# Kernel optimization log

Measured on AMD Instinct MI355X. Metric: run time of the kernel, lower is better.

The kernel has to match this reference:

```python
import jax, jax.numpy as jnp
import numpy as np

NUM_GROUPS = 32
EPS = 1e-5


def group_norm(x, w, b):
    # x: [B, C, H, W]
    B, C, H, W = x.shape
    g = x.reshape(B, NUM_GROUPS, C // NUM_GROUPS, H, W)
    mu = g.mean(axis=(2, 3, 4), keepdims=True)
    var = g.var(axis=(2, 3, 4), keepdims=True)
    g = (g - mu) * jax.lax.rsqrt(var + EPS)
    x = g.reshape(B, C, H, W)
    return x * w[None, :, None, None] + b[None, :, None, None]


def conv1x1(x, w, b):
    # 1x1 conv == channel matmul; x: [B, C, H, W], w: [O, C], b: [O]
    return jnp.einsum('bchw,oc->bohw', x, w) + b[None, :, None, None]


def setup_inputs() -> dict:
    key = jax.random.key(0)
    ks = jax.random.split(key, 11)
    C = 512
    B, H, W = 4, 64, 64
    s = 1.0 / np.sqrt(C)
    return {
        'x': jax.random.normal(ks[0], (B, C, H, W), jnp.float32),
        'gn_w': jax.random.uniform(ks[1], (C,), jnp.float32, 0.5, 1.5),
        'gn_b': jax.random.normal(ks[2], (C,), jnp.float32) * 0.1,
        'wq': jax.random.normal(ks[3], (C, C), jnp.float32) * s,
        'bq': jax.random.normal(ks[4], (C,), jnp.float32) * 0.01,
        'wk': jax.random.normal(ks[5], (C, C), jnp.float32) * s,
        'bk': jax.random.normal(ks[6], (C,), jnp.float32) * 0.01,
        'wv': jax.random.normal(ks[7], (C, C), jnp.float32) * s,
        'bv': jax.random.normal(ks[8], (C,), jnp.float32) * 0.01,
        'wo': jax.random.normal(ks[9], (C, C), jnp.float32) * s,
        'bo': jax.random.normal(ks[10], (C,), jnp.float32) * 0.01,
    }


def reference(x, gn_w, gn_b, wq, bq, wk, bk, wv, bv, wo, bo):
    B, C, H, W = x.shape
    h_ = group_norm(x, gn_w, gn_b)
    q = conv1x1(h_, wq, bq).reshape(B, C, H * W)   # [B, C, HW]
    k = conv1x1(h_, wk, bk).reshape(B, C, H * W)
    v = conv1x1(h_, wv, bv).reshape(B, C, H * W)
    # scores: q^T k, scaled by C^-0.5; softmax over keys
    scores = jnp.einsum('bci,bcj->bij', q, k) * (C ** -0.5)  # [B, HW, HW]
    attn = jax.nn.softmax(scores, axis=-1)
    # h_[b,c,i] = sum_j v[b,c,j] * attn[b,i,j]
    h_ = jnp.einsum('bcj,bij->bci', v, attn).reshape(B, C, H, W)
    return x + conv1x1(h_, wo, bo)
```

## Files before the change

kernel.cpp:

```cpp
#include <hip/hip_runtime.h>
#include <hip/hip_bf16.h>

typedef __attribute__((ext_vector_type(8))) __bf16 bf16x8;
typedef __attribute__((ext_vector_type(4))) float f32x4;

__device__ __forceinline__ unsigned short f2bf(float f) {
  union { float f; unsigned u; } v; v.f = f;
  unsigned r = v.u + 0x7fffu + ((v.u >> 16) & 1u);
  return (unsigned short)(r >> 16);
}

__device__ __forceinline__ void gload_lds16(const void* g, void* s) {
  __builtin_amdgcn_global_load_lds(
      (const __attribute__((address_space(1))) void*)g,
      (__attribute__((address_space(3))) void*)s, 16, 0, 0);
}

__global__ __launch_bounds__(256) void convert_w(
    const float* __restrict__ wq, const float* __restrict__ wk,
    const float* __restrict__ wv, const float* __restrict__ wo,
    unsigned short* __restrict__ dst) {
  const int m = blockIdx.x >> 10;
  const float* src = (m == 0) ? wq : (m == 1) ? wk : (m == 2) ? wv : wo;
  const int idx = ((blockIdx.x & 1023) << 8) | threadIdx.x;
  dst[m * 262144 + idx] = f2bf(src[idx]);
}

__global__ __launch_bounds__(256) void zero_k(float* __restrict__ p, int n) {
  const int i = blockIdx.x * 256 + threadIdx.x;
  if (i < n) p[i] = 0.f;
}

__global__ __launch_bounds__(256) void gn_stats(
    const float* __restrict__ x, float2* __restrict__ partials) {
  const int bg = blockIdx.x >> 2, part = blockIdx.x & 3;
  const float* xg = x + (size_t)bg * 65536 + part * 1024;
  const int t = threadIdx.x;
  float s = 0.f, ss = 0.f;
#pragma unroll
  for (int r = 0; r < 16; ++r) {
    const float4 v = *(const float4*)(xg + (size_t)r * 4096 + t * 4);
    s += v.x + v.y + v.z + v.w;
    ss += v.x * v.x + v.y * v.y + v.z * v.z + v.w * v.w;
  }
#pragma unroll
  for (int m = 32; m; m >>= 1) { s += __shfl_xor(s, m); ss += __shfl_xor(ss, m); }
  __shared__ float red[8];
  const int wave = t >> 6, lane = t & 63;
  if (lane == 0) { red[wave] = s; red[wave + 4] = ss; }
  __syncthreads();
  if (t == 0) {
    float2 p;
    p.x = red[0] + red[1] + red[2] + red[3];
    p.y = red[4] + red[5] + red[6] + red[7];
    partials[blockIdx.x] = p;
  }
}

__global__ __launch_bounds__(256) void gn_apply(
    const float* __restrict__ x, const float2* __restrict__ partials,
    const float* __restrict__ gw, const float* __restrict__ gb,
    unsigned short* __restrict__ h_t) {
  const int bg = blockIdx.x >> 3, cc = blockIdx.x & 7;
  const int b = bg >> 5, g = bg & 31;
  const int t = threadIdx.x;
  __shared__ float chs[32];
  __shared__ unsigned short tile[16][520];
  if (t < 16) {
    const float2 p0 = partials[bg * 4 + 0], p1 = partials[bg * 4 + 1];
    const float2 p2 = partials[bg * 4 + 2], p3 = partials[bg * 4 + 3];
    const float S = p0.x + p1.x + p2.x + p3.x;
    const float SS = p0.y + p1.y + p2.y + p3.y;
    const float mu = S * (1.f / 65536.f);
    const float rstd = rsqrtf(SS * (1.f / 65536.f) - mu * mu + 1e-5f);
    const float sc = gw[g * 16 + t] * rstd;
    chs[t] = sc;
    chs[16 + t] = gb[g * 16 + t] - mu * sc;
  }
  __syncthreads();
  const float* xg = x + (size_t)bg * 65536 + cc * 512;
#pragma unroll
  for (int rr = 0; rr < 8; ++rr) {
    const int r = rr * 2 + (t >> 7), i = (t & 127) * 4;
    const float4 v = *(const float4*)(xg + (size_t)r * 4096 + i);
    const float sc = chs[r], sh = chs[16 + r];
    ushort4 o;
    o.x = f2bf(v.x * sc + sh); o.y = f2bf(v.y * sc + sh);
    o.z = f2bf(v.z * sc + sh); o.w = f2bf(v.w * sc + sh);
    *(ushort4*)&tile[r][i] = o;
  }
  __syncthreads();
  unsigned short* outp = h_t + ((size_t)b * 4096 + cc * 512) * 512 + g * 16;
#pragma unroll
  for (int rep = 0; rep < 4; ++rep) {
    const int task = rep * 256 + t;
    const int nl = task >> 1, half = (task & 1) * 8;
    ushort4 o0, o1;
    o0.x = tile[half + 0][nl]; o0.y = tile[half + 1][nl];
    o0.z = tile[half + 2][nl]; o0.w = tile[half + 3][nl];
    o1.x = tile[half + 4][nl]; o1.y = tile[half + 5][nl];
    o1.z = tile[half + 6][nl]; o1.w = tile[half + 7][nl];
    *(ushort4*)(outp + (size_t)nl * 512 + half) = o0;
    *(ushort4*)(outp + (size_t)nl * 512 + half + 4) = o1;
  }
}

__global__ __launch_bounds__(256) void reduce4_k(
    const float* __restrict__ part, const float* __restrict__ l,
    unsigned short* __restrict__ dst) {
  const size_t i = ((size_t)blockIdx.x * 256 + threadIdx.x) * 4;
  f32x4 s0 = *(const f32x4*)(part + i);
  f32x4 s1 = *(const f32x4*)(part + 2097152 + i);
  f32x4 s2 = *(const f32x4*)(part + 4194304 + i);
  f32x4 s3 = *(const f32x4*)(part + 6291456 + i);
  f32x4 s = (s0 + s1) + (s2 + s3);
  const float inv = 1.f / l[i >> 9];
  ushort4 o;
  o.x = f2bf(s[0] * inv); o.y = f2bf(s[1] * inv);
  o.z = f2bf(s[2] * inv); o.w = f2bf(s[3] * inv);
  *(ushort4*)(dst + i) = o;
}

__global__ __launch_bounds__(512, 4) void gemm_s256(
    const unsigned short* __restrict__ A, const unsigned short* __restrict__ Bt,
    unsigned short* __restrict__ Out, float* __restrict__ lsum) {
  __shared__ __align__(16) char smem[73728];
  const int tid = threadIdx.x;
  const int wave = tid >> 6, lane = tid & 63;
  const int l15 = lane & 15, l4 = lane >> 4;
  const int wm = wave >> 1, wn = wave & 1;

  const int bz = blockIdx.z;
  A += (size_t)bz * 2097152;
  Bt += (size_t)bz * 2097152;
  Out += (size_t)bz * 16777216;
  lsum += (size_t)bz * 4096;

  const int id = blockIdx.y * 32 + blockIdx.x;
  const int xcd = id & 7, j = id >> 3;
  const int by = ((xcd >> 1) << 2) + (j >> 4);
  const int bx = ((xcd & 1) << 4) + (j & 15);
  const int row0 = by << 8, col0 = bx << 7;

  const int ar = tid >> 2;
  const int akc = (tid & 3) ^ ((tid >> 3) & 3);

  auto stage = [&](int kt, int bi) {
    const int kb = kt << 5;
    char* base = smem + bi * 24576;
    const unsigned short* gA = A + (size_t)(row0 + ar) * 512 + kb + akc * 8;
    const unsigned short* gB = Bt + (size_t)(col0 + ar) * 512 + kb + akc * 8;
    gload_lds16(gA, base + wave * 1024);
    gload_lds16(gA + (size_t)128 * 512, base + 8192 + wave * 1024);
    gload_lds16(gB, base + 16384 + wave * 1024);
  };

  f32x4 acc[4][4];
#pragma unroll
  for (int r = 0; r < 4; ++r)
#pragma unroll
    for (int c = 0; c < 4; ++c) acc[r][c] = (f32x4)0.f;

  const int xsw = (l4 ^ ((l15 >> 1) & 3)) << 4;

  auto compute = [&](int bi) {
    const char* pa = smem + bi * 24576 + (wm * 64 + l15) * 64 + xsw;
    const char* pb = smem + bi * 24576 + 16384 + (wn * 64 + l15) * 64 + xsw;
    bf16x8 af[4], bfr[4];
#pragma unroll
    for (int r = 0; r < 4; ++r) af[r] = *(const bf16x8*)(pa + r * 1024);
#pragma unroll
    for (int c = 0; c < 4; ++c) bfr[c] = *(const bf16x8*)(pb + c * 1024);
#pragma unroll
    for (int r = 0; r < 4; ++r)
#pragma unroll
      for (int c = 0; c < 4; ++c)
        acc[r][c] = __builtin_amdgcn_mfma_f32_16x16x32_bf16(af[r], bfr[c], acc[r][c], 0, 0, 0);
  };

  stage(0, 0);
  stage(1, 1);
  int bi = 0;
  for (int kt = 0; kt < 15; ++kt) {
    asm volatile("s_waitcnt vmcnt(3)" ::: "memory");
    __builtin_amdgcn_s_barrier();
    __builtin_amdgcn_sched_barrier(0);
    if (kt + 2 < 16) stage(kt + 2, (kt + 2) % 3);
    compute(bi);
    bi = (bi == 2) ? 0 : bi + 1;
  }
  asm volatile("s_waitcnt vmcnt(0)" ::: "memory");
  __builtin_amdgcn_s_barrier();
  __builtin_amdgcn_sched_barrier(0);
  compute(bi);

  __syncthreads();
  unsigned short* tile = (unsigned short*)smem;
#pragma unroll
  for (int c = 0; c < 4; ++c) {
    const int coll = wn * 64 + c * 16 + l15;
#pragma unroll
    for (int r = 0; r < 4; ++r) {
      const int rowl = wm * 64 + r * 16 + l4 * 4;
#pragma unroll
      for (int j = 0; j < 4; ++j)
        tile[(rowl + j) * 136 + coll] = f2bf(__expf(acc[r][c][j]));
    }
  }
  __syncthreads();
#pragma unroll
  for (int it = 0; it < 8; ++it) {
    const int idx = it * 512 + tid;
    const int rw = idx >> 4, ch = (idx & 15) * 8;
    const uint4 vv = *(const uint4*)&tile[rw * 136 + ch];
    *(uint4*)(Out + (size_t)(row0 + rw) * 4096 + col0 + ch) = vv;
    const unsigned* uu = (const unsigned*)&vv;
    float s = 0.f;
#pragma unroll
    for (int q = 0; q < 4; ++q) {
      union { unsigned u; float f; } w;
      w.u = uu[q] << 16; s += w.f;
      w.u = uu[q] & 0xffff0000u; s += w.f;
    }
    s += __shfl_xor(s, 1); s += __shfl_xor(s, 2);
    s += __shfl_xor(s, 4); s += __shfl_xor(s, 8);
    if ((lane & 15) == 0) atomicAdd(&lsum[row0 + rw], s);
  }
}

__global__ __launch_bounds__(512, 2) void gemm_pv(
    const unsigned short* __restrict__ P, const unsigned short* __restrict__ Vt,
    unsigned short* __restrict__ Out, const float* __restrict__ lrow) {
  __shared__ __align__(16) char smem[147456];
  const int tid = threadIdx.x;
  const int wave = tid >> 6, lane = tid & 63;
  const int l15 = lane & 15, l4 = lane >> 4;
  const int wm = wave >> 1, wn = wave & 1;

  const int L = blockIdx.x + ((blockIdx.y + (blockIdx.z << 4)) << 2);
  const int xcd = L & 7, j = L >> 3;
  const int panel = xcd * 8 + (j >> 2);
  const int bx = j & 3, by = panel & 15, bz = panel >> 4;
  const int row0 = by << 8, col0 = bx << 7;
  P += (size_t)bz * 16777216;
  Vt += (size_t)bz * 2097152;
  Out += (size_t)bz * 2097152;
  lrow += bz * 4096;

  const int sr = tid >> 3;
  const int sc8 = (tid & 7) ^ (sr & 7);
  const unsigned short* gA = P + (size_t)(row0 + sr) * 4096 + sc8 * 8;
  const unsigned short* gB = Vt + (size_t)(col0 + sr) * 4096 + sc8 * 8;

  auto stA = [&](int kt, int bi, int p) {
    gload_lds16(gA + (size_t)(p << 6) * 4096 + (kt << 6),
                smem + bi * 49152 + p * 8192 + wave * 1024);
  };
  auto stB = [&](int kt, int bi, int p) {
    gload_lds16(gB + (size_t)(p << 6) * 4096 + (kt << 6),
                smem + bi * 49152 + 32768 + p * 8192 + wave * 1024);
  };

  f32x4 acc[4][4];
#pragma unroll
  for (int r = 0; r < 4; ++r)
#pragma unroll
    for (int c = 0; c < 4; ++c) acc[r][c] = (f32x4)0.f;

  const int sw0 = (l4 ^ (l15 & 7)) << 4;
  const int sw1 = ((4 + l4) ^ (l15 & 7)) << 4;
  const int arow = (wm * 64 + l15) << 7;
  const int brow = (wn * 64 + l15) << 7;

  bf16x8 bfr[4][2];

  stA(0, 0, 0); stA(0, 0, 1); stA(0, 0, 2); stA(0, 0, 3);
  stB(0, 0, 0); stB(0, 0, 1);
  stA(1, 1, 0); stA(1, 1, 1); stA(1, 1, 2); stA(1, 1, 3);
  stB(1, 1, 0); stB(1, 1, 1);
  asm volatile("s_waitcnt vmcnt(6)" ::: "memory");
  __builtin_amdgcn_s_barrier();
  __builtin_amdgcn_sched_barrier(0);

  int bi = 0;
#pragma unroll 1
  for (int kt = 0; kt < 64; ++kt) {
    const char* bufA = smem + bi * 49152;
    const char* bufB = bufA + 32768;
    const int pb = (bi + 2) % 3;
    const bool pre = (kt + 2 < 64);
    bf16x8 a0, a1;
    a0 = *(const bf16x8*)(bufA + arow + sw0);
    a1 = *(const bf16x8*)(bufA + arow + sw1);
#pragma unroll
    for (int c = 0; c < 4; ++c) {
      bfr[c][0] = *(const bf16x8*)(bufB + brow + c * 2048 + sw0);
      bfr[c][1] = *(const bf16x8*)(bufB + brow + c * 2048 + sw1);
    }
    if (pre) { stA(kt + 2, pb, 0); stA(kt + 2, pb, 1); }
    __builtin_amdgcn_s_barrier();
    asm volatile("s_waitcnt lgkmcnt(0)" ::: "memory");
    __builtin_amdgcn_sched_barrier(0);
    __builtin_amdgcn_s_setprio(1);
#pragma unroll
    for (int c = 0; c < 4; ++c) {
      acc[0][c] = __builtin_amdgcn_mfma_f32_16x16x32_bf16(a0, bfr[c][0], acc[0][c], 0, 0, 0);
      acc[0][c] = __builtin_amdgcn_mfma_f32_16x16x32_bf16(a1, bfr[c][1], acc[0][c], 0, 0, 0);
    }
    __builtin_amdgcn_s_setprio(0);
    __builtin_amdgcn_s_barrier();
    a0 = *(const bf16x8*)(bufA + arow + 2048 + sw0);
    a1 = *(const bf16x8*)(bufA + arow + 2048 + sw1);
    if (pre) { stA(kt + 2, pb, 2); stA(kt + 2, pb, 3); }
    __builtin_amdgcn_s_barrier();
    asm volatile("s_waitcnt lgkmcnt(0)" ::: "memory");
    __builtin_amdgcn_sched_barrier(0);
    __builtin_amdgcn_s_setprio(1);
#pragma unroll
    for (int c = 0; c < 4; ++c) {
      acc[1][c] = __builtin_amdgcn_mfma_f32_16x16x32_bf16(a0, bfr[c][0], acc[1][c], 0, 0, 0);
      acc[1][c] = __builtin_amdgcn_mfma_f32_16x16x32_bf16(a1, bfr[c][1], acc[1][c], 0, 0, 0);
    }
    __builtin_amdgcn_s_setprio(0);
    __builtin_amdgcn_s_barrier();
    a0 = *(const bf16x8*)(bufA + arow + 4096 + sw0);
    a1 = *(const bf16x8*)(bufA + arow + 4096 + sw1);
    if (pre) { stB(kt + 2, pb, 0); stB(kt + 2, pb, 1); }
    __builtin_amdgcn_s_barrier();
    asm volatile("s_waitcnt lgkmcnt(0)" ::: "memory");
    __builtin_amdgcn_sched_barrier(0);
    __builtin_amdgcn_s_setprio(1);
#pragma unroll
    for (int c = 0; c < 4; ++c) {
      acc[2][c] = __builtin_amdgcn_mfma_f32_16x16x32_bf16(a0, bfr[c][0], acc[2][c], 0, 0, 0);
      acc[2][c] = __builtin_amdgcn_mfma_f32_16x16x32_bf16(a1, bfr[c][1], acc[2][c], 0, 0, 0);
    }
    __builtin_amdgcn_s_setprio(0);
    __builtin_amdgcn_s_barrier();
    a0 = *(const bf16x8*)(bufA + arow + 6144 + sw0);
    a1 = *(const bf16x8*)(bufA + arow + 6144 + sw1);
    __builtin_amdgcn_s_barrier();
    asm volatile("s_waitcnt lgkmcnt(0)" ::: "memory");
    __builtin_amdgcn_sched_barrier(0);
    __builtin_amdgcn_s_setprio(1);
#pragma unroll
    for (int c = 0; c < 4; ++c) {
      acc[3][c] = __builtin_amdgcn_mfma_f32_16x16x32_bf16(a0, bfr[c][0], acc[3][c], 0, 0, 0);
      acc[3][c] = __builtin_amdgcn_mfma_f32_16x16x32_bf16(a1, bfr[c][1], acc[3][c], 0, 0, 0);
    }
    __builtin_amdgcn_s_setprio(0);
    if (pre) asm volatile("s_waitcnt vmcnt(6)" ::: "memory");
    else     asm volatile("s_waitcnt vmcnt(0)" ::: "memory");
    __builtin_amdgcn_s_barrier();
    __builtin_amdgcn_sched_barrier(0);
    bi = (bi == 2) ? 0 : bi + 1;
  }

  __syncthreads();
  unsigned short* tile = (unsigned short*)smem;
#pragma unroll
  for (int c = 0; c < 4; ++c) {
    const int coll = wn * 64 + c * 16 + l15;
#pragma unroll
    for (int r = 0; r < 4; ++r) {
      const int rowl = wm * 64 + r * 16 + l4 * 4;
#pragma unroll
      for (int j = 0; j < 4; ++j) {
        const float v = acc[r][c][j] * (1.0f / lrow[row0 + rowl + j]);
        tile[(rowl + j) * 136 + coll] = f2bf(v);
      }
    }
  }
  __syncthreads();
#pragma unroll
  for (int it = 0; it < 8; ++it) {
    const int idx = it * 512 + tid;
    const int rw = idx >> 4, ch = (idx & 15) * 8;
    const uint4 vv = *(const uint4*)&tile[rw * 136 + ch];
    *(uint4*)(Out + (size_t)(row0 + rw) * 512 + col0 + ch) = vv;
  }
}

template <bool OUT_BF16, int BIAS_MODE, bool RESID, bool TRANS_OUT, int SWZ,
          bool COAL>
__global__ __launch_bounds__(256) void gemm_bt(
    const unsigned short* __restrict__ A, long long sA, int lda,
    const unsigned short* __restrict__ Bt, long long sB, int ldb,
    void* __restrict__ OutV, long long sO, int ldo,
    const float* __restrict__ bias,
    const float* __restrict__ resid, long long sR,
    int K, float scale) {
  __shared__ __align__(16) char smem[49152];
  const int tid = threadIdx.x;
  const int wave = tid >> 6, lane = tid & 63;
  const int l15 = lane & 15, l4 = lane >> 4;
  const int wm = wave >> 1, wn = wave & 1;

  int bx = blockIdx.x, by = blockIdx.y, bz = blockIdx.z;
  if constexpr (SWZ == 1) {
    const int id = by * 32 + bx;
    const int xcd = id & 7, j = id >> 3;
    by = ((xcd >> 1) << 3) + (j >> 4);
    bx = ((xcd & 1) << 4) + (j & 15);
  } else if constexpr (SWZ == 2) {
    const int L = bx + ((by + (bz << 5)) << 2);
    const int xcd = L & 7, j = L >> 3;
    const int pair = xcd * 16 + (j >> 2);
    bx = j & 3;
    by = pair & 31;
    bz = pair >> 5;
  }
  const int row0 = by << 7, col0 = bx << 7;
  A += (size_t)bz * sA;
  Bt += (size_t)bz * sB;
  if (RESID) resid += (size_t)bz * sR;
  if constexpr (BIAS_MODE == 3) bias += (size_t)bz * sR;
  char* outB = (char*)OutV + (size_t)bz * sO * (OUT_BF16 ? 2 : 4);

  const int ar = tid >> 2;
  const int akc = (tid & 3) ^ ((tid >> 3) & 3);

  auto stage = [&](int kt, int bi) {
    const int kb = kt << 5;
    char* sAl = smem + bi * 16384 + wave * 1024;
    char* sBl = sAl + 8192;
    const unsigned short* gA = A + (size_t)(row0 + ar) * lda + kb + akc * 8;
    const unsigned short* gB = Bt + (size_t)(col0 + ar) * ldb + kb + akc * 8;
    gload_lds16(gA, sAl);
    gload_lds16(gB, sBl);
    gload_lds16(gA + (size_t)64 * lda, sAl + 4096);
    gload_lds16(gB + (size_t)64 * ldb, sBl + 4096);
  };

  f32x4 acc[4][4];
#pragma unroll
  for (int r = 0; r < 4; ++r)
#pragma unroll
    for (int c = 0; c < 4; ++c) acc[r][c] = (f32x4)0.f;

  const int nk = K >> 5;
  const int xsw = (l4 ^ ((l15 >> 1) & 3)) << 4;

  auto compute = [&](int bi) {
    const char* pa = smem + bi * 16384 + (wm * 64 + l15) * 64 + xsw;
    const char* pb = smem + bi * 16384 + 8192 + (wn * 64 + l15) * 64 + xsw;
    bf16x8 af[4], bfr[4];
#pragma unroll
    for (int r = 0; r < 4; ++r) af[r] = *(const bf16x8*)(pa + r * 1024);
#pragma unroll
    for (int c = 0; c < 4; ++c) bfr[c] = *(const bf16x8*)(pb + c * 1024);
#pragma unroll
    for (int r = 0; r < 4; ++r)
#pragma unroll
      for (int c = 0; c < 4; ++c)
        acc[r][c] = __builtin_amdgcn_mfma_f32_16x16x32_bf16(af[r], bfr[c], acc[r][c], 0, 0, 0);
  };

  stage(0, 0);
  stage(1, 1);
  int bi = 0;
  for (int kt = 0; kt < nk - 1; ++kt) {
    asm volatile("s_waitcnt vmcnt(4)" ::: "memory");
    __builtin_amdgcn_s_barrier();
    __builtin_amdgcn_sched_barrier(0);
    if (kt + 2 < nk) stage(kt + 2, (kt + 2) % 3);
    compute(bi);
    bi = (bi == 2) ? 0 : bi + 1;
  }
  asm volatile("s_waitcnt vmcnt(0)" ::: "memory");
  __builtin_amdgcn_s_barrier();
  __builtin_amdgcn_sched_barrier(0);
  compute(bi);

  if constexpr (COAL && !TRANS_OUT) {
    __syncthreads();
    if constexpr (OUT_BF16) {
      unsigned short* tile = (unsigned short*)smem;
#pragma unroll
      for (int c = 0; c < 4; ++c) {
        const int coll = wn * 64 + c * 16 + l15;
        float badd = 0.f;
        if constexpr (BIAS_MODE == 1) badd = bias[col0 + coll];
#pragma unroll
        for (int r = 0; r < 4; ++r) {
          const int rowl = wm * 64 + r * 16 + l4 * 4;
#pragma unroll
          for (int j = 0; j < 4; ++j) {
            float v;
            if constexpr (BIAS_MODE == 3)
              v = acc[r][c][j] * (1.0f / bias[row0 + rowl + j]);
            else
              v = (acc[r][c][j] + badd) * scale;
            tile[(rowl + j) * 136 + coll] = f2bf(v);
          }
        }
      }
      __syncthreads();
      unsigned short* outp = (unsigned short*)outB;
#pragma unroll
      for (int it = 0; it < 8; ++it) {
        const int idx = it * 256 + tid;
        const int rw = idx >> 4, ch = (idx & 15) * 8;
        const uint4 vv = *(const uint4*)&tile[rw * 136 + ch];
        *(uint4*)(outp + (size_t)(row0 + rw) * ldo + col0 + ch) = vv;
      }
    } else {
      float* tile = (float*)smem;
#pragma unroll
      for (int p = 0; p < 2; ++p) {
        if (wm == p) {
#pragma unroll
          for (int c = 0; c < 4; ++c) {
            const int coll = wn * 64 + c * 16 + l15;
            float badd = 0.f;
            if constexpr (BIAS_MODE == 1) badd = bias[col0 + coll];
#pragma unroll
            for (int r = 0; r < 4; ++r) {
              const int rowl = r * 16 + l4 * 4;
#pragma unroll
              for (int j = 0; j < 4; ++j) {
                float v = acc[r][c][j] + badd;
                if constexpr (BIAS_MODE == 2) v += bias[row0 + p * 64 + rowl + j];
                tile[(rowl + j) * 132 + coll] = v * scale;
              }
            }
          }
        }
        __syncthreads();
        float* outp = (float*)outB;
#pragma unroll
        for (int it = 0; it < 8; ++it) {
          const int idx = it * 256 + tid;
          const int rw = idx >> 5, ch = (idx & 31) * 4;
          const int rowg = row0 + p * 64 + rw;
          f32x4 v = *(const f32x4*)&tile[rw * 132 + ch];
          if constexpr (RESID) {
            const float* rp = resid + (size_t)rowg * ldo + col0 + ch;
            v[0] += rp[0]; v[1] += rp[1]; v[2] += rp[2]; v[3] += rp[3];
          }
          *(f32x4*)(outp + (size_t)rowg * ldo + col0 + ch) = v;
        }
        __syncthreads();
      }
    }
  } else if constexpr (!TRANS_OUT) {
#pragma unroll
    for (int c = 0; c < 4; ++c) {
      const int colg = col0 + wn * 64 + c * 16 + l15;
      float badd = 0.f;
      if constexpr (BIAS_MODE == 1) badd = bias[colg];
#pragma unroll
      for (int r = 0; r < 4; ++r) {
        const int rowg = row0 + wm * 64 + r * 16 + l4 * 4;
#pragma unroll
        for (int j = 0; j < 4; ++j) {
          float v = acc[r][c][j] + badd;
          if constexpr (BIAS_MODE == 2) v += bias[rowg + j];
          v *= scale;
          if constexpr (RESID) v += resid[(size_t)(rowg + j) * ldo + colg];
          if constexpr (OUT_BF16)
            ((unsigned short*)outB)[(size_t)(rowg + j) * ldo + colg] = f2bf(v);
          else
            ((float*)outB)[(size_t)(rowg + j) * ldo + colg] = v;
        }
      }
    }
  } else {
    __syncthreads();
    unsigned short* tile = (unsigned short*)smem;
#pragma unroll
    for (int c = 0; c < 4; ++c) {
      const int coll = wn * 64 + c * 16 + l15;
      float badd = 0.f;
      if constexpr (BIAS_MODE == 1) badd = bias[col0 + coll];
#pragma unroll
      for (int r = 0; r < 4; ++r) {
        const int rowl = wm * 64 + r * 16 + l4 * 4;
#pragma unroll
        for (int j = 0; j < 4; ++j)
          tile[(rowl + j) * 132 + coll] = f2bf((acc[r][c][j] + badd) * scale);
      }
    }
    __syncthreads();
    unsigned short* outp = (unsigned short*)outB;
#pragma unroll 8
    for (int it = 0; it < 64; ++it) {
      const int idx = it * 256 + tid;
      const int cl = idx >> 7, il = idx & 127;
      outp[(size_t)(col0 + cl) * ldo + row0 + il] = tile[il * 132 + cl];
    }
  }
}

extern "C" void kernel_launch(void* const* d_in, const int* in_sizes, int n_in,
                              void* d_out, int out_size, void* d_ws, size_t ws_size,
                              hipStream_t stream) {
  const float* x   = (const float*)d_in[0];
  const float* gnw = (const float*)d_in[1];
  const float* gnb = (const float*)d_in[2];
  const float* wq  = (const float*)d_in[3];
  const float* bq  = (const float*)d_in[4];
  const float* wk  = (const float*)d_in[5];
  const float* bk  = (const float*)d_in[6];
  const float* wv  = (const float*)d_in[7];
  const float* bv  = (const float*)d_in[8];
  const float* wo  = (const float*)d_in[9];
  const float* bo  = (const float*)d_in[10];
  float* out = (float*)d_out;
  char* ws = (char*)d_ws;

  const size_t MB = 1u << 20;
  float2*         gnp  = (float2*)ws;
  float*          lrow = (float*)(ws + 64 * 1024);
  unsigned short* wbf  = (unsigned short*)(ws + 1 * MB);
  unsigned short* h_t  = (unsigned short*)(ws + 3 * MB);
  unsigned short* q_t  = (unsigned short*)(ws + 19 * MB);
  unsigned short* k_t  = (unsigned short*)(ws + 35 * MB);
  unsigned short* v_ct = (unsigned short*)(ws + 51 * MB);
  unsigned short* h2_t = (unsigned short*)(ws + 67 * MB);
  unsigned short* Pbuf = (unsigned short*)(ws + 83 * MB);
  float*          part = (float*)(ws + 115 * MB);

  const long long BS = 2097152;
  const long long PBS = 16777216;
  const float qscale = 0.044194173824159216f;
  const bool batched = ws_size >= 212 * MB;

  convert_w<<<dim3(4096), dim3(256), 0, stream>>>(wq, wk, wv, wo, wbf);
  gn_stats<<<dim3(512), dim3(256), 0, stream>>>(x, gnp);
  gn_apply<<<dim3(1024), dim3(256), 0, stream>>>(x, gnp, gnw, gnb, h_t);

  gemm_bt<true, 1, false, false, 0, true><<<dim3(4, 32, 4), 256, 0, stream>>>(
      h_t, BS, 512, wbf + 0, 0, 512, q_t, BS, 512, bq, nullptr, 0, 512, qscale);
  gemm_bt<true, 1, false, false, 0, true><<<dim3(4, 32, 4), 256, 0, stream>>>(
      h_t, BS, 512, wbf + 262144, 0, 512, k_t, BS, 512, bk, nullptr, 0, 512, 1.0f);
  gemm_bt<true, 1, false, true, 0, false><<<dim3(4, 32, 4), 256, 0, stream>>>(
      h_t, BS, 512, wbf + 524288, 0, 512, v_ct, BS, 4096, bv, nullptr, 0, 512, 1.0f);

  if (batched) {
    zero_k<<<dim3(64), dim3(256), 0, stream>>>(lrow, 16384);
    gemm_s256<<<dim3(32, 16, 4), dim3(512), 0, stream>>>(q_t, k_t, Pbuf, lrow);
    gemm_pv<<<dim3(4, 16, 4), dim3(512), 0, stream>>>(Pbuf, v_ct, h2_t, lrow);
  } else {
    for (int b = 0; b < 4; ++b) {
      zero_k<<<dim3(16), dim3(256), 0, stream>>>(lrow, 4096);
      gemm_s256<<<dim3(32, 16, 1), dim3(512), 0, stream>>>(
          q_t + (size_t)b * BS, k_t + (size_t)b * BS, Pbuf, lrow);
      gemm_bt<false, 0, false, false, 0, true><<<dim3(4, 32, 4), 256, 0, stream>>>(
          Pbuf, 1024, 4096, v_ct + (size_t)b * BS, 1024, 4096,
          part, 2097152, 512, nullptr, nullptr, 0, 1024, 1.0f);
      reduce4_k<<<dim3(2048), dim3(256), 0, stream>>>(part, lrow, h2_t + (size_t)b * BS);
    }
  }

  gemm_bt<false, 2, true, false, 0, true><<<dim3(32, 4, 4), 256, 0, stream>>>(
      wbf + 786432, 0, 512, h2_t, BS, 512, out, BS, 4096, bo, x, BS, 512, 1.0f);
}
```

Before: 268.4 us.

## Fuse Q/K/V projections into one GEMM launch and fold lrow zeroing into weight conversion

Replaces three separate gemm_bt launches for the Q, K and V 1x1 projections with one gemm_qkv kernel over a 12x32x4 grid. Each block picks its weight slice and epilogue (scaled Q, K, or transposed V) from blockIdx.x. It also moves the zeroing of the softmax row-sum buffer into extra blocks of convert_w, dropping the zero_k launch. The aim is fewer launches and tail gaps, and a larger single grid to fill the CUs. The cost is a hand-written GEMM with its own triple-buffered pipeline and a strided scalar transposed store for V.

```diff
diff --git a/kernel.cpp b/kernel.cpp
--- a/kernel.cpp
+++ b/kernel.cpp
@@ -19,7 +19,11 @@
 __global__ __launch_bounds__(256) void convert_w(
     const float* __restrict__ wq, const float* __restrict__ wk,
     const float* __restrict__ wv, const float* __restrict__ wo,
-    unsigned short* __restrict__ dst) {
+    unsigned short* __restrict__ dst, float* __restrict__ lrow) {
+  if (blockIdx.x >= 4096) {
+    lrow[((blockIdx.x - 4096) << 8) | threadIdx.x] = 0.f;
+    return;
+  }
   const int m = blockIdx.x >> 10;
   const float* src = (m == 0) ? wq : (m == 1) ? wk : (m == 2) ? wv : wo;
   const int idx = ((blockIdx.x & 1023) << 8) | threadIdx.x;
@@ -121,6 +125,130 @@
   *(ushort4*)(dst + i) = o;
 }
 
+__global__ __launch_bounds__(256) void gemm_qkv(
+    const unsigned short* __restrict__ H, const unsigned short* __restrict__ W,
+    unsigned short* __restrict__ q_t, unsigned short* __restrict__ k_t,
+    unsigned short* __restrict__ v_ct,
+    const float* __restrict__ bq, const float* __restrict__ bk,
+    const float* __restrict__ bv, float qscale) {
+  __shared__ __align__(16) char smem[49152];
+  const int tid = threadIdx.x;
+  const int wave = tid >> 6, lane = tid & 63;
+  const int l15 = lane & 15, l4 = lane >> 4;
+  const int wm = wave >> 1, wn = wave & 1;
+
+  const int bx = blockIdx.x, by = blockIdx.y, bz = blockIdx.z;
+  const int mode = bx >> 2;
+  const int colv = (bx & 3) << 7;
+  const int row0 = by << 7;
+  const unsigned short* A = H + (size_t)bz * 2097152;
+  const unsigned short* Bt = W + (size_t)bx * 65536;
+
+  const int ar = tid >> 2;
+  const int akc = (tid & 3) ^ ((tid >> 3) & 3);
+
+  auto stage = [&](int kt, int bi) {
+    const int kb = kt << 5;
+    char* sAl = smem + bi * 16384 + wave * 1024;
+    char* sBl = sAl + 8192;
+    const unsigned short* gA = A + (size_t)(row0 + ar) * 512 + kb + akc * 8;
+    const unsigned short* gB = Bt + (size_t)ar * 512 + kb + akc * 8;
+    gload_lds16(gA, sAl);
+    gload_lds16(gB, sBl);
+    gload_lds16(gA + (size_t)64 * 512, sAl + 4096);
+    gload_lds16(gB + (size_t)64 * 512, sBl + 4096);
+  };
+
+  f32x4 acc[4][4];
+#pragma unroll
+  for (int r = 0; r < 4; ++r)
+#pragma unroll
+    for (int c = 0; c < 4; ++c) acc[r][c] = (f32x4)0.f;
+
+  const int xsw = (l4 ^ ((l15 >> 1) & 3)) << 4;
+
+  auto compute = [&](int bi) {
+    const char* pa = smem + bi * 16384 + (wm * 64 + l15) * 64 + xsw;
+    const char* pb = smem + bi * 16384 + 8192 + (wn * 64 + l15) * 64 + xsw;
+    bf16x8 af[4], bfr[4];
+#pragma unroll
+    for (int r = 0; r < 4; ++r) af[r] = *(const bf16x8*)(pa + r * 1024);
+#pragma unroll
+    for (int c = 0; c < 4; ++c) bfr[c] = *(const bf16x8*)(pb + c * 1024);
+#pragma unroll
+    for (int r = 0; r < 4; ++r)
+#pragma unroll
+      for (int c = 0; c < 4; ++c)
+        acc[r][c] = __builtin_amdgcn_mfma_f32_16x16x32_bf16(af[r], bfr[c], acc[r][c], 0, 0, 0);
+  };
+
+  stage(0, 0);
+  stage(1, 1);
+  int bi = 0;
+  for (int kt = 0; kt < 15; ++kt) {
+    asm volatile("s_waitcnt vmcnt(4)" ::: "memory");
+    __builtin_amdgcn_s_barrier();
+    __builtin_amdgcn_sched_barrier(0);
+    if (kt + 2 < 16) stage(kt + 2, (kt + 2) % 3);
+    compute(bi);
+    bi = (bi == 2) ? 0 : bi + 1;
+  }
+  asm volatile("s_waitcnt vmcnt(0)" ::: "memory");
+  __builtin_amdgcn_s_barrier();
+  __builtin_amdgcn_sched_barrier(0);
+  compute(bi);
+
+  const float* bias = (mode == 0) ? bq : (mode == 1) ? bk : bv;
+  const float scale = (mode == 0) ? qscale : 1.0f;
+  __syncthreads();
+  if (mode < 2) {
+    unsigned short* outp = ((mode == 0) ? q_t : k_t) + (size_t)bz * 2097152;
+    unsigned short* tile = (unsigned short*)smem;
+#pragma unroll
+    for (int c = 0; c < 4; ++c) {
+      const int coll = wn * 64 + c * 16 + l15;
+      const float badd = bias[colv + coll];
+#pragma unroll
+      for (int r = 0; r < 4; ++r) {
+        const int rowl = wm * 64 + r * 16 + l4 * 4;
+#pragma unroll
+        for (int j = 0; j < 4; ++j)
+          tile[(rowl + j) * 136 + coll] = f2bf((acc[r][c][j] + badd) * scale);
+      }
+    }
+    __syncthreads();
+#pragma unroll
+    for (int it = 0; it < 8; ++it) {
+      const int idx = it * 256 + tid;
+      const int rw = idx >> 4, ch = (idx & 15) * 8;
+      const uint4 vv = *(const uint4*)&tile[rw * 136 + ch];
+      *(uint4*)(outp + (size_t)(row0 + rw) * 512 + colv + ch) = vv;
+    }
+  } else {
+    unsigned short* outp = v_ct + (size_t)bz * 2097152;
+    unsigned short* tile = (unsigned short*)smem;
+#pragma unroll
+    for (int c = 0; c < 4; ++c) {
+      const int coll = wn * 64 + c * 16 + l15;
+      const float badd = bias[colv + coll];
+#pragma unroll
+      for (int r = 0; r < 4; ++r) {
+        const int rowl = wm * 64 + r * 16 + l4 * 4;
+#pragma unroll
+        for (int j = 0; j < 4; ++j)
+          tile[(rowl + j) * 132 + coll] = f2bf(acc[r][c][j] + badd);
+      }
+    }
+    __syncthreads();
+#pragma unroll 8
+    for (int it = 0; it < 64; ++it) {
+      const int idx = it * 256 + tid;
+      const int cl = idx >> 7, il = idx & 127;
+      outp[(size_t)(colv + cl) * 4096 + row0 + il] = tile[il * 132 + cl];
+    }
+  }
+}
+
 __global__ __launch_bounds__(512, 4) void gemm_s256(
     const unsigned short* __restrict__ A, const unsigned short* __restrict__ Bt,
     unsigned short* __restrict__ Out, float* __restrict__ lsum) {
@@ -622,23 +750,17 @@
   float*          part = (float*)(ws + 115 * MB);
 
   const long long BS = 2097152;
-  const long long PBS = 16777216;
   const float qscale = 0.044194173824159216f;
   const bool batched = ws_size >= 212 * MB;
 
-  convert_w<<<dim3(4096), dim3(256), 0, stream>>>(wq, wk, wv, wo, wbf);
+  convert_w<<<dim3(4160), dim3(256), 0, stream>>>(wq, wk, wv, wo, wbf, lrow);
   gn_stats<<<dim3(512), dim3(256), 0, stream>>>(x, gnp);
   gn_apply<<<dim3(1024), dim3(256), 0, stream>>>(x, gnp, gnw, gnb, h_t);
 
-  gemm_bt<true, 1, false, false, 0, true><<<dim3(4, 32, 4), 256, 0, stream>>>(
-      h_t, BS, 512, wbf + 0, 0, 512, q_t, BS, 512, bq, nullptr, 0, 512, qscale);
-  gemm_bt<true, 1, false, false, 0, true><<<dim3(4, 32, 4), 256, 0, stream>>>(
-      h_t, BS, 512, wbf + 262144, 0, 512, k_t, BS, 512, bk, nullptr, 0, 512, 1.0f);
-  gemm_bt<true, 1, false, true, 0, false><<<dim3(4, 32, 4), 256, 0, stream>>>(
-      h_t, BS, 512, wbf + 524288, 0, 512, v_ct, BS, 4096, bv, nullptr, 0, 512, 1.0f);
+  gemm_qkv<<<dim3(12, 32, 4), dim3(256), 0, stream>>>(
+      h_t, wbf, q_t, k_t, v_ct, bq, bk, bv, qscale);
 
   if (batched) {
-    zero_k<<<dim3(64), dim3(256), 0, stream>>>(lrow, 16384);
     gemm_s256<<<dim3(32, 16, 4), dim3(512), 0, stream>>>(q_t, k_t, Pbuf, lrow);
     gemm_pv<<<dim3(4, 16, 4), dim3(512), 0, stream>>>(Pbuf, v_ct, h2_t, lrow);
   } else {
```

Result: faster. 249.0 us (-7.2%).
